# Optimization experiments

Hardware: AMD Instinct MI355X
Metric: run time of the kernel (lower is better)

The kernel has to match this reference:

```python
import jax, jax.numpy as jnp
import numpy as np
from jax import lax

B, T, V, E, H, DA, R, S, A, NR = 256, 64, 30000, 300, 512, 350, 16, 64, 16, 3


def setup_inputs() -> dict:
    key = jax.random.key(0)
    ks = jax.random.split(key, 24)

    def gn(k, shape, scale):
        return (jax.random.normal(k, shape) * scale).astype(jnp.float32)

    def xavier(k, shape):
        fan = sum(shape[-2:]) if len(shape) >= 2 else shape[0] * 2
        return (jax.random.uniform(k, shape, minval=-1.0, maxval=1.0)
                * np.sqrt(6.0 / fan)).astype(jnp.float32)

    s = 1.0 / np.sqrt(H)
    inp = {
        "tokens": jax.random.randint(ks[0], (B, T), 0, V),
        "lengths": jnp.full((B,), T, dtype=jnp.int32),
        "embedding": gn(ks[1], (V, E), 0.02),
        # BiLSTM layer 0 (input E), layer 1 (input 2H); gates order i,f,g,o (PyTorch)
        "Wih_l0f": gn(ks[2], (4 * H, E), s), "Whh_l0f": gn(ks[3], (4 * H, H), s), "b_l0f": jnp.zeros((4 * H,), jnp.float32),
        "Wih_l0b": gn(ks[4], (4 * H, E), s), "Whh_l0b": gn(ks[5], (4 * H, H), s), "b_l0b": jnp.zeros((4 * H,), jnp.float32),
        "Wih_l1f": gn(ks[6], (4 * H, 2 * H), s), "Whh_l1f": gn(ks[7], (4 * H, H), s), "b_l1f": jnp.zeros((4 * H,), jnp.float32),
        "Wih_l1b": gn(ks[8], (4 * H, 2 * H), s), "Whh_l1b": gn(ks[9], (4 * H, H), s), "b_l1b": jnp.zeros((4 * H,), jnp.float32),
        "ws1": xavier(ks[10], (DA, 2 * H)),
        "ws2": xavier(ks[11], (R, DA)),
        "caps_W": xavier(ks[12], (R, 2 * H, S * A)),
    }
    return inp


def _lstm_dir(x, Wih, Whh, b, reverse=False):
    # x: [T, B, D] -> hidden states [T, B, H]
    if reverse:
        x = x[::-1]
    h0 = jnp.zeros((x.shape[1], Whh.shape[1]), x.dtype)
    c0 = jnp.zeros_like(h0)

    def step(carry, xt):
        h, c = carry
        z = xt @ Wih.T + h @ Whh.T + b
        i, f, g, o = jnp.split(z, 4, axis=-1)
        c = jax.nn.sigmoid(f) * c + jax.nn.sigmoid(i) * jnp.tanh(g)
        h = jax.nn.sigmoid(o) * jnp.tanh(c)
        return (h, c), h

    _, hs = lax.scan(step, (h0, c0), x)
    return hs[::-1] if reverse else hs


def reference(tokens, lengths, embedding,
              Wih_l0f, Whh_l0f, b_l0f, Wih_l0b, Whh_l0b, b_l0b,
              Wih_l1f, Whh_l1f, b_l1f, Wih_l1b, Whh_l1b, b_l1b,
              ws1, ws2, caps_W):
    # Embedding + 2-layer BiLSTM (all lengths == T, so packing is a no-op).
    x = embedding[tokens].transpose(1, 0, 2)          # [T, B, E]
    l0 = jnp.concatenate([_lstm_dir(x, Wih_l0f, Whh_l0f, b_l0f),
                          _lstm_dir(x, Wih_l0b, Whh_l0b, b_l0b, True)], -1)
    l1 = jnp.concatenate([_lstm_dir(l0, Wih_l1f, Whh_l1f, b_l1f),
                          _lstm_dir(l0, Wih_l1b, Whh_l1b, b_l1b, True)], -1)
    outp = l1.transpose(1, 0, 2)                      # [B, T, 2H]

    # Self-attention pooling (note: original applies NO softmax on alphas).
    hbar = jnp.tanh(jnp.einsum('bte,ae->bta', outp, ws1))   # [B, T, DA]
    alphas = jnp.einsum('bta,ra->btr', hbar, ws2)           # [B, T, R]
    attention = alphas.transpose(0, 2, 1)                   # [B, R, T]
    sent = jnp.einsum('brt,bte->bre', attention, outp)      # [B, R, 2H]

    # Capsule votes + dynamic routing.
    votes = jnp.einsum('bri,rio->bro', sent, caps_W).reshape(B, R, S, A)
    logits = jnp.zeros((B, R, S), votes.dtype)
    for _ in range(NR):
        route = jax.nn.softmax(logits, axis=2)
        preact = jnp.einsum('brs,brsa->bsa', route, votes)  # [B, S, A]
        norm = jnp.linalg.norm(preact, axis=2, keepdims=True)
        act = preact / norm * (norm * norm / (0.5 + norm * norm))
        logits = logits + jnp.einsum('brsa,bsa->brs', votes, act)
    class_logits = jnp.linalg.norm(act, axis=-1)            # [B, S]
    return (sent, class_logits)
```

## Files before the change

kernel.cpp:

```cpp
#include <hip/hip_runtime.h>
#include <stdint.h>

#define PB 256
#define PT 64
#define PE 300
#define PH 512
#define PDA 350
#define PR 16
#define PS 64
#define PA 16

typedef __attribute__((ext_vector_type(8))) short short8;
typedef __attribute__((ext_vector_type(4))) float f4;
typedef unsigned long long u64;

__device__ __forceinline__ float bf2f(unsigned short u) {
    unsigned v = ((unsigned)u) << 16;
    return __builtin_bit_cast(float, v);
}
__device__ __forceinline__ unsigned short f2bf(float f) {
    unsigned u = __builtin_bit_cast(unsigned int, f);
    u = u + 0x7fffu + ((u >> 16) & 1u);
    return (unsigned short)(u >> 16);
}
__device__ __forceinline__ float sigf(float x) { return 1.f / (1.f + __expf(-x)); }
__device__ __forceinline__ float tanhf_(float x) { return 1.f - 2.f / (1.f + __expf(2.f * x)); }


__global__ __launch_bounds__(256) void k_embed(const int* __restrict__ tokens,
                                               const float* __restrict__ emb,
                                               unsigned short* __restrict__ X) {
    int idx = blockIdx.x * 256 + threadIdx.x;
    if (idx >= 16384 * 320) return;
    int row = idx / 320, e = idx - row * 320;
    int t = row >> 8, b = row & 255;
    float v = 0.f;
    if (e < 300) v = emb[(long)tokens[b * 64 + t] * 300 + e];
    X[idx] = f2bf(v);
}

__global__ __launch_bounds__(256) void k_cvt_pad(const float* __restrict__ src,
                                                 unsigned short* __restrict__ dst,
                                                 int N, int K, int N2, int K2) {
    int idx = blockIdx.x * 256 + threadIdx.x;
    if (idx >= N2 * K2) return;
    int n = idx / K2, k = idx - n * K2;
    float v = (n < N && k < K) ? src[(long)n * K + k] : 0.f;
    dst[idx] = f2bf(v);
}

__global__ __launch_bounds__(256) void k_capsT(const float* __restrict__ src,
                                               unsigned short* __restrict__ dst) {
    __shared__ float tile[32][33];
    int r = blockIdx.x, kb = blockIdx.y * 32, nb = blockIdx.z * 32;
    int tx = threadIdx.x & 31, ty = threadIdx.x >> 5;
    for (int i = 0; i < 32; i += 8)
        tile[ty + i][tx] = src[((long)r << 20) + (long)(kb + ty + i) * 1024 + nb + tx];
    __syncthreads();
    for (int i = 0; i < 32; i += 8)
        dst[((long)r << 20) + (long)(nb + ty + i) * 1024 + kb + tx] = f2bf(tile[tx][ty + i]);
}

__global__ __launch_bounds__(256) void k_whh_shuf(const float* __restrict__ W,
                                                  unsigned short* __restrict__ dst) {
    int idx = blockIdx.x * 256 + threadIdx.x;
    int el = idx & 7, lane = (idx >> 3) & 63, ks = (idx >> 9) & 15, nt = (idx >> 13) & 7, hs = idx >> 16;
    int gcol = (nt >> 1) * 512 + hs * 32 + (nt & 1) * 16 + (lane & 15);
    int k = ks * 32 + (lane >> 4) * 8 + el;
    dst[idx] = f2bf(W[(long)gcol * 512 + k]);
}

template <int OUT_BF16, int TANH>
__global__ __launch_bounds__(256) void k_gemm(const unsigned short* __restrict__ A,
                                              const unsigned short* __restrict__ W,
                                              void* __restrict__ Cv,
                                              const float* __restrict__ bias,
                                              int K, int lda, int ldc,
                                              long aOffZ, long wOffZ, long cOffZ, long bOffZ) {
    A += blockIdx.z * aOffZ;
    W += blockIdx.z * wOffZ;
    if (bias) bias += blockIdx.z * bOffZ;
    const long cbase = blockIdx.z * cOffZ;
    const int m0 = blockIdx.x * 128, n0 = blockIdx.y * 128;
    __shared__ unsigned short As[4096], Bs[4096];
    const int w = threadIdx.x >> 6, l = threadIdx.x & 63;
    const int wm = w & 1, wn = w >> 1;
    const int fr = l & 15, fk = (l >> 4) * 8;
    f4 acc[4][4] = {};
    for (int k0 = 0; k0 < K; k0 += 32) {
        __syncthreads();
#pragma unroll
        for (int i = 0; i < 2; i++) {
            int tI = w + i * 4;
            const unsigned short* ga = A + (long)(m0 + tI * 16 + fr) * lda + k0 + fk;
            const unsigned short* gb = W + (long)(n0 + tI * 16 + fr) * K + k0 + fk;
            *(short8*)&As[tI * 512 + l * 8] = *(const short8*)ga;
            *(short8*)&Bs[tI * 512 + l * 8] = *(const short8*)gb;
        }
        __syncthreads();
        short8 av[4], bv[4];
#pragma unroll
        for (int mt = 0; mt < 4; mt++) av[mt] = *(short8*)&As[(wm * 4 + mt) * 512 + l * 8];
#pragma unroll
        for (int nt = 0; nt < 4; nt++) bv[nt] = *(short8*)&Bs[(wn * 4 + nt) * 512 + l * 8];
#pragma unroll
        for (int mt = 0; mt < 4; mt++)
#pragma unroll
            for (int nt = 0; nt < 4; nt++)
                acc[mt][nt] = __builtin_amdgcn_mfma_f32_16x16x32_bf16(av[mt], bv[nt], acc[mt][nt], 0, 0, 0);
    }
#pragma unroll
    for (int mt = 0; mt < 4; mt++) {
        int row = m0 + wm * 64 + mt * 16 + (l >> 4) * 4;
#pragma unroll
        for (int nt = 0; nt < 4; nt++) {
            int col = n0 + wn * 64 + nt * 16 + (l & 15);
            float bb = bias ? bias[col] : 0.f;
#pragma unroll
            for (int i = 0; i < 4; i++) {
                float v = acc[mt][nt][i] + bb;
                if (TANH) v = tanhf_(v);
                long off = cbase + (long)(row + i) * ldc + col;
                if (OUT_BF16)
                    ((unsigned short*)Cv)[off] = f2bf(v);
                else
                    ((float*)Cv)[off] = v;
            }
        }
    }
}

__global__ __launch_bounds__(256) void k_lstm(const unsigned short* __restrict__ Zx,
                                              const unsigned short* __restrict__ Wshuf,
                                              unsigned short* __restrict__ hsteps,
                                              unsigned short* __restrict__ Lout,
                                              unsigned* __restrict__ cnt) {
    extern __shared__ char smem[];
    unsigned short* Wl = (unsigned short*)smem;
    float* zl = (float*)(smem + 131072);
    const int bid = blockIdx.x;
    const int dir = bid >> 6, bg = (bid >> 4) & 3, hs = bid & 15;
    const int tid = threadIdx.x;
    const int l = tid & 63;
    const int w = tid >> 6;
    const int mt2 = w & 1, hc2 = w >> 1;

    {
        const short8* src = (const short8*)(Wshuf + ((long)(dir * 16 + hs) << 16));
        short8* dst = (short8*)Wl;
        for (int i = tid; i < 8192; i += 256) dst[i] = src[i];
    }
    {
        unsigned short* hz = hsteps + (long)dir * (256 * 512);
        for (int i = tid; i < 1024; i += 256) {
            int r = i >> 4, c2 = i & 15;
            __hip_atomic_store((unsigned*)&hz[(bg * 64 + r) * 512 + hs * 32 + c2 * 2], 0u,
                               __ATOMIC_RELAXED, __HIP_MEMORY_SCOPE_AGENT);
        }
    }
    unsigned* myc = cnt + (dir * 4 + bg) * 32;
    asm volatile("s_waitcnt vmcnt(0)" ::: "memory");
    __syncthreads();
    if (tid == 0) __hip_atomic_fetch_add(myc, 1u, __ATOMIC_RELAXED, __HIP_MEMORY_SCOPE_AGENT);

    float c_reg[8];
#pragma unroll
    for (int i = 0; i < 8; i++) c_reg[i] = 0.f;

    const int pw_r[2] = { tid >> 4, 16 + (tid >> 4) };
    const int pw_c0 = (tid & 15) * 2;

    for (int step = 0; step < 64; step++) {
        const int t_eff = dir ? (63 - step) : step;
        const unsigned short* zbase = Zx + ((long)dir * 16384 + (long)t_eff * 256) * 2048;

        unsigned zpre[2][2][4];
#pragma unroll
        for (int half = 0; half < 2; half++)
#pragma unroll
            for (int k2 = 0; k2 < 2; k2++) {
                int rowg = bg * 64 + half * 32 + pw_r[k2];
                int jg = hs * 32 + pw_c0;
                const unsigned short* zrow = zbase + (long)rowg * 2048;
#pragma unroll
                for (int g = 0; g < 4; g++)
                    zpre[half][k2][g] = *(const unsigned*)&zrow[g * 512 + jg];
            }

        if (tid == 0) {
            unsigned target = 16u * (unsigned)(step + 1);
            while (__hip_atomic_load(myc, __ATOMIC_RELAXED, __HIP_MEMORY_SCOPE_AGENT) < target) {}
        }
        __syncthreads();

        f4 acc[2][4] = {};
        const unsigned short* hb = hsteps + ((long)step * 2 + dir) * (256 * 512);
        const unsigned short* pa0 = hb + (bg * 64 + (mt2 * 2 + 0) * 16 + (l & 15)) * 512 + (l >> 4) * 8;
        const unsigned short* pa1 = hb + (bg * 64 + (mt2 * 2 + 1) * 16 + (l & 15)) * 512 + (l >> 4) * 8;
        short8 a0 = *(const short8*)pa0;
        short8 a1 = *(const short8*)pa1;
#pragma unroll
        for (int ks = 0; ks < 16; ks++) {
            short8 a0c = a0, a1c = a1;
            if (ks < 15) {
                a0 = *(const short8*)(pa0 + (ks + 1) * 32);
                a1 = *(const short8*)(pa1 + (ks + 1) * 32);
            }
#pragma unroll
            for (int s = 0; s < 4; s++) {
                int nt = s * 2 + hc2;
                short8 b = *(short8*)&Wl[((nt * 16 + ks) * 64 + l) * 8];
                acc[0][s] = __builtin_amdgcn_mfma_f32_16x16x32_bf16(a0c, b, acc[0][s], 0, 0, 0);
                acc[1][s] = __builtin_amdgcn_mfma_f32_16x16x32_bf16(a1c, b, acc[1][s], 0, 0, 0);
            }
        }

        unsigned short* hw = hsteps + ((long)(step + 1) * 2 + dir) * (256 * 512);
#pragma unroll
        for (int half = 0; half < 2; half++) {
            __syncthreads();
            if (mt2 == half) {
#pragma unroll
                for (int i2 = 0; i2 < 2; i2++) {
                    int rloc = i2 * 16 + (l >> 4) * 4;
#pragma unroll
                    for (int s = 0; s < 4; s++) {
                        int col = s * 32 + hc2 * 16 + (l & 15);
#pragma unroll
                        for (int i = 0; i < 4; i++) zl[(rloc + i) * 132 + col] = acc[i2][s][i];
                    }
                }
            }
            __syncthreads();
#pragma unroll
            for (int k2 = 0; k2 < 2; k2++) {
                int r = pw_r[k2];
                int c0 = pw_c0;
                int rowg = bg * 64 + half * 32 + r;
                int jg = hs * 32 + c0;
                unsigned ui = zpre[half][k2][0], uf = zpre[half][k2][1];
                unsigned ug = zpre[half][k2][2], uo = zpre[half][k2][3];
                float zi0 = zl[r * 132 + 0 * 32 + c0] + bf2f((unsigned short)ui);
                float zf0 = zl[r * 132 + 1 * 32 + c0] + bf2f((unsigned short)uf);
                float zg0 = zl[r * 132 + 2 * 32 + c0] + bf2f((unsigned short)ug);
                float zo0 = zl[r * 132 + 3 * 32 + c0] + bf2f((unsigned short)uo);
                float zi1 = zl[r * 132 + 0 * 32 + c0 + 1] + bf2f((unsigned short)(ui >> 16));
                float zf1 = zl[r * 132 + 1 * 32 + c0 + 1] + bf2f((unsigned short)(uf >> 16));
                float zg1 = zl[r * 132 + 2 * 32 + c0 + 1] + bf2f((unsigned short)(ug >> 16));
                float zo1 = zl[r * 132 + 3 * 32 + c0 + 1] + bf2f((unsigned short)(uo >> 16));
                int ci = half * 4 + k2 * 2;
                float ca = sigf(zf0) * c_reg[ci] + sigf(zi0) * tanhf_(zg0);
                c_reg[ci] = ca;
                float ha = sigf(zo0) * tanhf_(ca);
                float cb = sigf(zf1) * c_reg[ci + 1] + sigf(zi1) * tanhf_(zg1);
                c_reg[ci + 1] = cb;
                float hbv = sigf(zo1) * tanhf_(cb);
                unsigned pack = (unsigned)f2bf(ha) | ((unsigned)f2bf(hbv) << 16);
                __hip_atomic_store((unsigned*)&hw[(long)rowg * 512 + jg], pack,
                                   __ATOMIC_RELAXED, __HIP_MEMORY_SCOPE_AGENT);
                *(unsigned*)&Lout[((long)t_eff * 256 + rowg) * 1024 + dir * 512 + jg] = pack;
            }
        }
        asm volatile("s_waitcnt vmcnt(0)" ::: "memory");
        __syncthreads();
        if (tid == 0) __hip_atomic_fetch_add(myc, 1u, __ATOMIC_RELAXED, __HIP_MEMORY_SCOPE_AGENT);
    }
}

__global__ __launch_bounds__(256) void k_alphas(const unsigned short* __restrict__ hbar,
                                                const unsigned short* __restrict__ ws2,
                                                float* __restrict__ att) {
    int w = threadIdx.x >> 6, l = threadIdx.x & 63;
    int mtile = blockIdx.x * 4 + w;
    f4 acc = {};
    const unsigned short* arow = hbar + (long)(mtile * 16 + (l & 15)) * 384 + (l >> 4) * 8;
    const unsigned short* brow = ws2 + (long)(l & 15) * 384 + (l >> 4) * 8;
    for (int ks = 0; ks < 12; ks++) {
        short8 a = *(const short8*)&arow[ks * 32];
        short8 b = *(const short8*)&brow[ks * 32];
        acc = __builtin_amdgcn_mfma_f32_16x16x32_bf16(a, b, acc, 0, 0, 0);
    }
    int r = l & 15;
#pragma unroll
    for (int i = 0; i < 4; i++) {
        int bt = mtile * 16 + (l >> 4) * 4 + i;
        int b = bt & 255, t = bt >> 8;
        att[((long)b * 16 + r) * 64 + t] = acc[i];
    }
}

__global__ __launch_bounds__(256) void k_sent(const float* __restrict__ att,
                                              const unsigned short* __restrict__ L1,
                                              float* __restrict__ sent,
                                              unsigned short* __restrict__ sentb) {
    int b = blockIdx.x, n0 = blockIdx.y * 128;
    __shared__ float al[1024];
    for (int i = threadIdx.x; i < 1024; i += 256) al[i] = att[(long)b * 1024 + i];
    __syncthreads();
    int n = n0 + (threadIdx.x & 127);
    int rh = (threadIdx.x >> 7) * 8;
    float acc[8] = {};
    for (int t = 0; t < 64; t++) {
        float x = bf2f(L1[((long)t * 256 + b) * 1024 + n]);
#pragma unroll
        for (int r = 0; r < 8; r++) acc[r] += al[(rh + r) * 64 + t] * x;
    }
#pragma unroll
    for (int r = 0; r < 8; r++) {
        long o = ((long)b * 16 + rh + r) * 1024 + n;
        sent[o] = acc[r];
        sentb[o] = f2bf(acc[r]);
    }
}

__global__ __launch_bounds__(256) void k_route(const float* __restrict__ votes,
                                               float* __restrict__ clog) {
    __shared__ float v[16384];
    __shared__ float logits[1024];
    __shared__ float route[1024];
    __shared__ float pre[1024];
    __shared__ float act[1024];
    __shared__ float cl[64];
    int b = blockIdx.x, tid = threadIdx.x;
    for (int i = tid; i < 4096; i += 256) ((f4*)v)[i] = ((const f4*)(votes + (long)b * 16384))[i];
    for (int i = tid; i < 1024; i += 256) logits[i] = 0.f;
    __syncthreads();
    for (int it = 0; it < 3; it++) {
        if (tid < 16) {
            float m = -1e30f;
            for (int s = 0; s < 64; s++) m = fmaxf(m, logits[tid * 64 + s]);
            float sum = 0.f;
            for (int s = 0; s < 64; s++) {
                float e = __expf(logits[tid * 64 + s] - m);
                route[tid * 64 + s] = e;
                sum += e;
            }
            float inv = 1.f / sum;
            for (int s = 0; s < 64; s++) route[tid * 64 + s] *= inv;
        }
        __syncthreads();
#pragma unroll
        for (int k = 0; k < 4; k++) {
            int p = k * 256 + tid;
            int s = p >> 4, a = p & 15;
            float acc = 0.f;
            for (int r = 0; r < 16; r++) acc += route[r * 64 + s] * v[(r * 64 + s) * 16 + a];
            pre[p] = acc;
        }
        __syncthreads();
        if (tid < 64) {
            float nsq = 0.f;
            for (int a = 0; a < 16; a++) nsq += pre[tid * 16 + a] * pre[tid * 16 + a];
            float norm = sqrtf(nsq);
            float sc = norm / (0.5f + nsq);
            for (int a = 0; a < 16; a++) act[tid * 16 + a] = pre[tid * 16 + a] * sc;
            cl[tid] = nsq / (0.5f + nsq);
        }
        __syncthreads();
#pragma unroll
        for (int k = 0; k < 4; k++) {
            int p = k * 256 + tid;
            int r = p >> 6, s = p & 63;
            float acc = 0.f;
            for (int a = 0; a < 16; a++) acc += v[(r * 64 + s) * 16 + a] * act[s * 16 + a];
            logits[p] += acc;
        }
        __syncthreads();
    }
    if (tid < 64) clog[(long)b * 64 + tid] = cl[tid];
}

extern "C" void kernel_launch(void* const* d_in, const int* in_sizes, int n_in,
                              void* d_out, int out_size, void* d_ws, size_t ws_size,
                              hipStream_t stream) {
    const int* tokens = (const int*)d_in[0];
    const float* embedding = (const float*)d_in[2];
    const float* Wih_l0f = (const float*)d_in[3];
    const float* Whh_l0f = (const float*)d_in[4];
    const float* b_l0f = (const float*)d_in[5];
    const float* Wih_l0b = (const float*)d_in[6];
    const float* Whh_l0b = (const float*)d_in[7];
    const float* b_l0b = (const float*)d_in[8];
    const float* Wih_l1f = (const float*)d_in[9];
    const float* Whh_l1f = (const float*)d_in[10];
    const float* b_l1f = (const float*)d_in[11];
    const float* Wih_l1b = (const float*)d_in[12];
    const float* Whh_l1b = (const float*)d_in[13];
    const float* b_l1b = (const float*)d_in[14];
    const float* ws1 = (const float*)d_in[15];
    const float* ws2 = (const float*)d_in[16];
    const float* caps_W = (const float*)d_in[17];
    float* out = (float*)d_out;

    char* ws = (char*)d_ws;
    size_t o = 0;
    unsigned short* Xb16 = (unsigned short*)(ws + o); o += (size_t)16384 * 320 * 2;
    unsigned short* ZxL = (unsigned short*)(ws + o); size_t zx_off = o; o += (size_t)2 * 16384 * 2048 * 2;
    unsigned short* L0 = (unsigned short*)(ws + o); o += (size_t)16384 * 1024 * 2;
    unsigned short* L1 = (unsigned short*)(ws + o); o += (size_t)16384 * 1024 * 2;
    unsigned short* Wl0b = (unsigned short*)(ws + o); o += (size_t)2 * 2048 * 320 * 2;
    unsigned short* Wl1b = (unsigned short*)(ws + o); o += (size_t)2 * 2048 * 1024 * 2;
    unsigned short* Wsh0 = (unsigned short*)(ws + o); o += (size_t)2 * 1048576 * 2;
    unsigned short* Wsh1 = (unsigned short*)(ws + o); o += (size_t)2 * 1048576 * 2;
    unsigned short* ws1b = (unsigned short*)(ws + o); o += (size_t)384 * 1024 * 2;
    unsigned short* ws2b = (unsigned short*)(ws + o); o += (size_t)16 * 384 * 2 + 192;
    float* biasc = (float*)(ws + o); o += (size_t)4 * 2048 * 4;
    unsigned* cnts = (unsigned*)(ws + o); o += 4096;
    unsigned short* hsteps = (unsigned short*)(ws + o);
    unsigned short* capsT = (unsigned short*)(ws + o);
    o += (size_t)65 * 2 * 256 * 512 * 2;
    unsigned short* hbarb = (unsigned short*)(ws + zx_off);
    float* att = (float*)(ws + zx_off + (size_t)16384 * 384 * 2);
    unsigned short* sentb = (unsigned short*)(ws + zx_off + (size_t)16384 * 384 * 2 + 1048576);
    float* votes = (float*)(ws + zx_off + (size_t)16384 * 384 * 2 + 1048576 + (size_t)256 * 16 * 1024 * 2);

    hipMemsetAsync(cnts, 0, 4096, stream);

    k_embed<<<16384 * 320 / 256, 256, 0, stream>>>(tokens, embedding, Xb16);
    k_cvt_pad<<<(2048 * 320 + 255) / 256, 256, 0, stream>>>(Wih_l0f, Wl0b, 2048, 300, 2048, 320);
    k_cvt_pad<<<(2048 * 320 + 255) / 256, 256, 0, stream>>>(Wih_l0b, Wl0b + (size_t)2048 * 320, 2048, 300, 2048, 320);
    k_cvt_pad<<<(2048 * 1024 + 255) / 256, 256, 0, stream>>>(Wih_l1f, Wl1b, 2048, 1024, 2048, 1024);
    k_cvt_pad<<<(2048 * 1024 + 255) / 256, 256, 0, stream>>>(Wih_l1b, Wl1b + (size_t)2048 * 1024, 2048, 1024, 2048, 1024);
    k_cvt_pad<<<(384 * 1024 + 255) / 256, 256, 0, stream>>>(ws1, ws1b, 350, 1024, 384, 1024);
    k_cvt_pad<<<(16 * 384 + 255) / 256, 256, 0, stream>>>(ws2, ws2b, 16, 350, 16, 384);
    k_whh_shuf<<<4096, 256, 0, stream>>>(Whh_l0f, Wsh0);
    k_whh_shuf<<<4096, 256, 0, stream>>>(Whh_l0b, Wsh0 + 1048576);
    k_whh_shuf<<<4096, 256, 0, stream>>>(Whh_l1f, Wsh1);
    k_whh_shuf<<<4096, 256, 0, stream>>>(Whh_l1b, Wsh1 + 1048576);
    hipMemcpyAsync(biasc + 0, b_l0f, 2048 * 4, hipMemcpyDeviceToDevice, stream);
    hipMemcpyAsync(biasc + 2048, b_l0b, 2048 * 4, hipMemcpyDeviceToDevice, stream);
    hipMemcpyAsync(biasc + 4096, b_l1f, 2048 * 4, hipMemcpyDeviceToDevice, stream);
    hipMemcpyAsync(biasc + 6144, b_l1b, 2048 * 4, hipMemcpyDeviceToDevice, stream);

    hipFuncSetAttribute(reinterpret_cast<const void*>(k_lstm),
                        hipFuncAttributeMaxDynamicSharedMemorySize, 147968);

    k_gemm<1, 0><<<dim3(128, 16, 2), 256, 0, stream>>>(
        Xb16, Wl0b, ZxL, biasc, 320, 320, 2048,
        0L, (long)2048 * 320, (long)16384 * 2048, 2048L);
    k_lstm<<<128, 256, 147968, stream>>>(ZxL, Wsh0, hsteps, L0, cnts);
    k_gemm<1, 0><<<dim3(128, 16, 2), 256, 0, stream>>>(
        L0, Wl1b, ZxL, biasc + 4096, 1024, 1024, 2048,
        0L, (long)2048 * 1024, (long)16384 * 2048, 2048L);
    k_lstm<<<128, 256, 147968, stream>>>(ZxL, Wsh1, hsteps, L1, cnts + 256);
    k_capsT<<<dim3(16, 32, 32), 256, 0, stream>>>(caps_W, capsT);
    k_gemm<1, 1><<<dim3(128, 3, 1), 256, 0, stream>>>(
        L1, ws1b, hbarb, nullptr, 1024, 1024, 384, 0L, 0L, 0L, 0L);
    k_alphas<<<256, 256, 0, stream>>>(hbarb, ws2b, att);
    k_sent<<<dim3(256, 8), 256, 0, stream>>>(att, L1, out, sentb);
    k_gemm<0, 0><<<dim3(2, 8, 16), 256, 0, stream>>>(
        sentb, capsT, votes, nullptr, 1024, 16384, 16384,
        1024L, 1048576L, 1024L, 0L);
    k_route<<<256, 256, 0, stream>>>(votes, out + (size_t)4194304);
}
```

Before: 1.755 ms.

## Compute LSTM gates directly from MFMA accumulators, drop LDS staging and barriers

The LSTM recurrence kernel no longer stages MFMA accumulators through shared memory for the gate epilogue. Each lane now applies the cell update directly to its own accumulator elements, whose layout already matches the gate order. This removes four __syncthreads per step and the 16KB LDS scratch buffer. It also issues all 32 h-state loads up front before the MFMA loop, and defers the Lout output stores until after the step's counter increment so they sit off the critical path. In exchange it uses more registers and replaces packed 32-bit stores and loads with scalar 16-bit ones.

```diff
diff --git a/kernel.cpp b/kernel.cpp
--- a/kernel.cpp
+++ b/kernel.cpp
@@ -130,14 +130,13 @@
     }
 }
 
-__global__ __launch_bounds__(256) void k_lstm(const unsigned short* __restrict__ Zx,
-                                              const unsigned short* __restrict__ Wshuf,
-                                              unsigned short* __restrict__ hsteps,
-                                              unsigned short* __restrict__ Lout,
-                                              unsigned* __restrict__ cnt) {
+__global__ __launch_bounds__(256, 1) void k_lstm(const unsigned short* __restrict__ Zx,
+                                                 const unsigned short* __restrict__ Wshuf,
+                                                 unsigned short* __restrict__ hsteps,
+                                                 unsigned short* __restrict__ Lout,
+                                                 unsigned* __restrict__ cnt) {
     extern __shared__ char smem[];
     unsigned short* Wl = (unsigned short*)smem;
-    float* zl = (float*)(smem + 131072);
     const int bid = blockIdx.x;
     const int dir = bid >> 6, bg = (bid >> 4) & 3, hs = bid & 15;
     const int tid = threadIdx.x;
@@ -167,24 +166,26 @@
 #pragma unroll
     for (int i = 0; i < 8; i++) c_reg[i] = 0.f;
 
-    const int pw_r[2] = { tid >> 4, 16 + (tid >> 4) };
-    const int pw_c0 = (tid & 15) * 2;
+    const int jg = hs * 32 + hc2 * 16 + (l & 15);
+    int rowg_[2][4];
+#pragma unroll
+    for (int i2 = 0; i2 < 2; i2++)
+#pragma unroll
+        for (int i = 0; i < 4; i++)
+            rowg_[i2][i] = bg * 64 + (mt2 * 2 + i2) * 16 + (l >> 4) * 4 + i;
 
     for (int step = 0; step < 64; step++) {
         const int t_eff = dir ? (63 - step) : step;
         const unsigned short* zbase = Zx + ((long)dir * 16384 + (long)t_eff * 256) * 2048;
 
-        unsigned zpre[2][2][4];
-#pragma unroll
-        for (int half = 0; half < 2; half++)
-#pragma unroll
-            for (int k2 = 0; k2 < 2; k2++) {
-                int rowg = bg * 64 + half * 32 + pw_r[k2];
-                int jg = hs * 32 + pw_c0;
-                const unsigned short* zrow = zbase + (long)rowg * 2048;
-#pragma unroll
-                for (int g = 0; g < 4; g++)
-                    zpre[half][k2][g] = *(const unsigned*)&zrow[g * 512 + jg];
+        unsigned short zpre[2][4][4];
+#pragma unroll
+        for (int i2 = 0; i2 < 2; i2++)
+#pragma unroll
+            for (int i = 0; i < 4; i++) {
+                const unsigned short* zrow = zbase + (long)rowg_[i2][i] * 2048 + jg;
+#pragma unroll
+                for (int g = 0; g < 4; g++) zpre[i2][i][g] = zrow[g * 512];
             }
 
         if (tid == 0) {
@@ -193,77 +194,57 @@
         }
         __syncthreads();
 
-        f4 acc[2][4] = {};
         const unsigned short* hb = hsteps + ((long)step * 2 + dir) * (256 * 512);
         const unsigned short* pa0 = hb + (bg * 64 + (mt2 * 2 + 0) * 16 + (l & 15)) * 512 + (l >> 4) * 8;
         const unsigned short* pa1 = hb + (bg * 64 + (mt2 * 2 + 1) * 16 + (l & 15)) * 512 + (l >> 4) * 8;
-        short8 a0 = *(const short8*)pa0;
-        short8 a1 = *(const short8*)pa1;
+        short8 a0[16], a1[16];
 #pragma unroll
         for (int ks = 0; ks < 16; ks++) {
-            short8 a0c = a0, a1c = a1;
-            if (ks < 15) {
-                a0 = *(const short8*)(pa0 + (ks + 1) * 32);
-                a1 = *(const short8*)(pa1 + (ks + 1) * 32);
-            }
+            a0[ks] = *(const short8*)(pa0 + ks * 32);
+            a1[ks] = *(const short8*)(pa1 + ks * 32);
+        }
+        asm volatile("" ::: "memory");
+
+        f4 acc[2][4] = {};
+#pragma unroll
+        for (int ks = 0; ks < 16; ks++) {
 #pragma unroll
             for (int s = 0; s < 4; s++) {
                 int nt = s * 2 + hc2;
                 short8 b = *(short8*)&Wl[((nt * 16 + ks) * 64 + l) * 8];
-                acc[0][s] = __builtin_amdgcn_mfma_f32_16x16x32_bf16(a0c, b, acc[0][s], 0, 0, 0);
-                acc[1][s] = __builtin_amdgcn_mfma_f32_16x16x32_bf16(a1c, b, acc[1][s], 0, 0, 0);
+                acc[0][s] = __builtin_amdgcn_mfma_f32_16x16x32_bf16(a0[ks], b, acc[0][s], 0, 0, 0);
+                acc[1][s] = __builtin_amdgcn_mfma_f32_16x16x32_bf16(a1[ks], b, acc[1][s], 0, 0, 0);
             }
         }
 
+        unsigned short hv[2][4];
         unsigned short* hw = hsteps + ((long)(step + 1) * 2 + dir) * (256 * 512);
 #pragma unroll
-        for (int half = 0; half < 2; half++) {
-            __syncthreads();
-            if (mt2 == half) {
-#pragma unroll
-                for (int i2 = 0; i2 < 2; i2++) {
-                    int rloc = i2 * 16 + (l >> 4) * 4;
-#pragma unroll
-                    for (int s = 0; s < 4; s++) {
-                        int col = s * 32 + hc2 * 16 + (l & 15);
-#pragma unroll
-                        for (int i = 0; i < 4; i++) zl[(rloc + i) * 132 + col] = acc[i2][s][i];
-                    }
-                }
+        for (int i2 = 0; i2 < 2; i2++)
+#pragma unroll
+            for (int i = 0; i < 4; i++) {
+                float zi = acc[i2][0][i] + bf2f(zpre[i2][i][0]);
+                float zf = acc[i2][1][i] + bf2f(zpre[i2][i][1]);
+                float zg = acc[i2][2][i] + bf2f(zpre[i2][i][2]);
+                float zo = acc[i2][3][i] + bf2f(zpre[i2][i][3]);
+                int ci = i2 * 4 + i;
+                float c = sigf(zf) * c_reg[ci] + sigf(zi) * tanhf_(zg);
+                c_reg[ci] = c;
+                float h = sigf(zo) * tanhf_(c);
+                unsigned short hb16 = f2bf(h);
+                hv[i2][i] = hb16;
+                __hip_atomic_store(&hw[(long)rowg_[i2][i] * 512 + jg], hb16,
+                                   __ATOMIC_RELAXED, __HIP_MEMORY_SCOPE_AGENT);
             }
-            __syncthreads();
-#pragma unroll
-            for (int k2 = 0; k2 < 2; k2++) {
-                int r = pw_r[k2];
-                int c0 = pw_c0;
-                int rowg = bg * 64 + half * 32 + r;
-                int jg = hs * 32 + c0;
-                unsigned ui = zpre[half][k2][0], uf = zpre[half][k2][1];
-                unsigned ug = zpre[half][k2][2], uo = zpre[half][k2][3];
-                float zi0 = zl[r * 132 + 0 * 32 + c0] + bf2f((unsigned short)ui);
-                float zf0 = zl[r * 132 + 1 * 32 + c0] + bf2f((unsigned short)uf);
-                float zg0 = zl[r * 132 + 2 * 32 + c0] + bf2f((unsigned short)ug);
-                float zo0 = zl[r * 132 + 3 * 32 + c0] + bf2f((unsigned short)uo);
-                float zi1 = zl[r * 132 + 0 * 32 + c0 + 1] + bf2f((unsigned short)(ui >> 16));
-                float zf1 = zl[r * 132 + 1 * 32 + c0 + 1] + bf2f((unsigned short)(uf >> 16));
-                float zg1 = zl[r * 132 + 2 * 32 + c0 + 1] + bf2f((unsigned short)(ug >> 16));
-                float zo1 = zl[r * 132 + 3 * 32 + c0 + 1] + bf2f((unsigned short)(uo >> 16));
-                int ci = half * 4 + k2 * 2;
-                float ca = sigf(zf0) * c_reg[ci] + sigf(zi0) * tanhf_(zg0);
-                c_reg[ci] = ca;
-                float ha = sigf(zo0) * tanhf_(ca);
-                float cb = sigf(zf1) * c_reg[ci + 1] + sigf(zi1) * tanhf_(zg1);
-                c_reg[ci + 1] = cb;
-                float hbv = sigf(zo1) * tanhf_(cb);
-                unsigned pack = (unsigned)f2bf(ha) | ((unsigned)f2bf(hbv) << 16);
-                __hip_atomic_store((unsigned*)&hw[(long)rowg * 512 + jg], pack,
-                                   __ATOMIC_RELAXED, __HIP_MEMORY_SCOPE_AGENT);
-                *(unsigned*)&Lout[((long)t_eff * 256 + rowg) * 1024 + dir * 512 + jg] = pack;
-            }
-        }
         asm volatile("s_waitcnt vmcnt(0)" ::: "memory");
         __syncthreads();
         if (tid == 0) __hip_atomic_fetch_add(myc, 1u, __ATOMIC_RELAXED, __HIP_MEMORY_SCOPE_AGENT);
+
+#pragma unroll
+        for (int i2 = 0; i2 < 2; i2++)
+#pragma unroll
+            for (int i = 0; i < 4; i++)
+                Lout[((long)t_eff * 256 + rowg_[i2][i]) * 1024 + dir * 512 + jg] = hv[i2][i];
     }
 }
 
@@ -433,16 +414,16 @@
     hipMemcpyAsync(biasc + 6144, b_l1b, 2048 * 4, hipMemcpyDeviceToDevice, stream);
 
     hipFuncSetAttribute(reinterpret_cast<const void*>(k_lstm),
-                        hipFuncAttributeMaxDynamicSharedMemorySize, 147968);
+                        hipFuncAttributeMaxDynamicSharedMemorySize, 131072);
 
     k_gemm<1, 0><<<dim3(128, 16, 2), 256, 0, stream>>>(
         Xb16, Wl0b, ZxL, biasc, 320, 320, 2048,
         0L, (long)2048 * 320, (long)16384 * 2048, 2048L);
-    k_lstm<<<128, 256, 147968, stream>>>(ZxL, Wsh0, hsteps, L0, cnts);
+    k_lstm<<<128, 256, 131072, stream>>>(ZxL, Wsh0, hsteps, L0, cnts);
     k_gemm<1, 0><<<dim3(128, 16, 2), 256, 0, stream>>>(
         L0, Wl1b, ZxL, biasc + 4096, 1024, 1024, 2048,
         0L, (long)2048 * 1024, (long)16384 * 2048, 2048L);
-    k_lstm<<<128, 256, 147968, stream>>>(ZxL, Wsh1, hsteps, L1, cnts + 256);
+    k_lstm<<<128, 256, 131072, stream>>>(ZxL, Wsh1, hsteps, L1, cnts + 256);
     k_capsT<<<dim3(16, 32, 32), 256, 0, stream>>>(caps_W, capsT);
     k_gemm<1, 1><<<dim3(128, 3, 1), 256, 0, stream>>>(
         L1, ws1b, hbarb, nullptr, 1024, 1024, 384, 0L, 0L, 0L, 0L);
```

New measurement: 1.785 ms. No clear change (+1.7%).
